# Kernel tuning notes

Hardware: AMD Instinct MI355X
Metric: run time of the kernel (lower is better)

Reference implementation:

```python
import jax, jax.numpy as jnp
import numpy as np

B, T, I, H, O = 1024, 512, 64, 256, 1

def setup_inputs() -> dict:
    key = jax.random.key(0)
    ks = jax.random.split(key, 12)
    s_ih0 = 1.0 / np.sqrt(H)
    def u(k, shape):
        return jax.random.uniform(k, shape, jnp.float32, -s_ih0, s_ih0)
    return {
        "x": jax.random.normal(ks[0], (B, T, I), jnp.float32),
        "w_ih0": u(ks[1], (4 * H, I)),
        "w_hh0": u(ks[2], (4 * H, H)),
        "b_ih0": u(ks[3], (4 * H,)),
        "b_hh0": u(ks[4], (4 * H,)),
        "w_ih1": u(ks[5], (4 * H, H)),
        "w_hh1": u(ks[6], (4 * H, H)),
        "b_ih1": u(ks[7], (4 * H,)),
        "b_hh1": u(ks[8], (4 * H,)),
        "fc_w": u(ks[9], (O, H)),
        "fc_b": u(ks[10], (O,)),
    }

def _lstm_layer(x, w_ih, w_hh, b_ih, b_hh):
    # x: [B, T, D_in] -> hidden sequence [B, T, H], gate order i,f,g,o (PyTorch)
    b, t, _ = x.shape
    h_dim = w_hh.shape[1]
    # precompute input projections for all timesteps: [T, B, 4H]
    xproj = (jnp.einsum('bti,gi->btg', x, w_ih) + b_ih + b_hh).transpose(1, 0, 2)
    h0 = jnp.zeros((b, h_dim), x.dtype)
    c0 = jnp.zeros((b, h_dim), x.dtype)

    def step(carry, xp):
        h, c = carry
        gates = xp + h @ w_hh.T  # [B, 4H]
        i_g, f_g, g_g, o_g = jnp.split(gates, 4, axis=-1)
        i_g = jax.nn.sigmoid(i_g)
        f_g = jax.nn.sigmoid(f_g)
        g_g = jnp.tanh(g_g)
        o_g = jax.nn.sigmoid(o_g)
        c = f_g * c + i_g * g_g
        h = o_g * jnp.tanh(c)
        return (h, c), h

    (h_last, _), hs = jax.lax.scan(step, (h0, c0), xproj)
    return hs.transpose(1, 0, 2), h_last

def reference(x, w_ih0, w_hh0, b_ih0, b_hh0, w_ih1, w_hh1, b_ih1, b_hh1, fc_w, fc_b):
    # Layer 0 -> (eval mode: dropout is identity) -> Layer 1 -> fc on last step
    h_seq0, _ = _lstm_layer(x, w_ih0, w_hh0, b_ih0, b_hh0)
    _, h_last1 = _lstm_layer(h_seq0, w_ih1, w_hh1, b_ih1, b_hh1)
    return h_last1 @ fc_w.T + fc_b  # [B, O]
```

## Files before the change

kernel.cpp:

```cpp
#include <hip/hip_runtime.h>
#include <stdint.h>


#define T_STEPS 512
#define NC0 10
#define NC1 16
#define WSLICE_ELEMS (4*(NC0+NC1)*512)
#define L1_OFF (4*NC0*512)
#define HN (1024*256)

typedef __attribute__((ext_vector_type(8))) short short8;
typedef __attribute__((ext_vector_type(4))) float floatx4;

__device__ __forceinline__ uint32_t f2bf(float f){
  uint32_t u = __builtin_bit_cast(uint32_t, f);
  return (u + 0x7fffu + ((u >> 16) & 1u)) >> 16;
}
__device__ __forceinline__ float bf2f(uint32_t b){
  return __builtin_bit_cast(float, b << 16);
}
__device__ __forceinline__ float sigm(float x){
  return __builtin_amdgcn_rcpf(1.0f + __builtin_amdgcn_exp2f(-1.44269504f*x));
}
__device__ __forceinline__ float tanhf_(float x){
  return 1.0f - 2.0f*__builtin_amdgcn_rcpf(1.0f + __builtin_amdgcn_exp2f(2.88539008f*x));
}
__device__ __forceinline__ floatx4 splat4(float v){ return (floatx4){v,v,v,v}; }

__device__ __forceinline__ void cvt8(const floatx4& v0, const floatx4& v1, short8& hi, short8& lo){
  #pragma unroll
  for (int j = 0; j < 8; ++j){
    float f = (j < 4) ? v0[j] : v1[j-4];
    uint32_t hb = f2bf(f); float fh = bf2f(hb); uint32_t lb = f2bf(f - fh);
    hi[j] = (short)hb; lo[j] = (short)lb;
  }
}

__device__ __forceinline__ short8 load_coh16(const uint16_t* p){
  short8 r;
  asm volatile("global_load_dwordx4 %0, %1, off sc0 sc1" : "=v"(r) : "v"(p));
  return r;
}
__device__ __forceinline__ floatx4 load_g16f(const float* p){
  floatx4 r;
  asm volatile("global_load_dwordx4 %0, %1, off" : "=v"(r) : "v"(p));
  return r;
}
__device__ __forceinline__ void store_coh2(uint16_t* p, uint32_t v){
  asm volatile("global_store_short %0, %1, off sc0 sc1" :: "v"(p), "v"(v) : "memory");
}
#define VM_WAIT(N) do{ asm volatile("s_waitcnt vmcnt(" #N ")" ::: "memory"); \
                       __builtin_amdgcn_sched_barrier(0); }while(0)

extern "C" __global__ void prep_weights(const float* __restrict__ wih0, const float* __restrict__ whh0,
                                        const float* __restrict__ wih1, const float* __restrict__ whh1,
                                        uint16_t* __restrict__ wfrag)
{
  int idx = blockIdx.x*256 + threadIdx.x;
  int s  = idx / WSLICE_ELEMS;
  int r  = idx - s*WSLICE_ELEMS;
  int layer = (r >= L1_OFF) ? 1 : 0;
  int rr = layer ? (r - L1_OFF) : r;
  int nc = layer ? NC1 : NC0;
  int n  = rr / (nc*512);
  int c  = (rr / 512) % nc;
  int l  = (rr >> 3) & 63;
  int j  = rr & 7;
  int k  = c*32 + ((l >> 4) << 3) + j;
  int grow = n*256 + s*16 + (l & 15);
  float v;
  if (!layer) v = (k < 64)  ? wih0[grow*64  + k] : whh0[grow*256 + (k - 64)];
  else        v = (k < 256) ? wih1[grow*256 + k] : whh1[grow*256 + (k - 256)];
  wfrag[idx] = (uint16_t)f2bf(v);
}

extern "C" __global__ void prep_bias(const float* __restrict__ bih0, const float* __restrict__ bhh0,
                                     const float* __restrict__ bih1, const float* __restrict__ bhh1,
                                     float* __restrict__ biasg)
{
  int idx = blockIdx.x*256 + threadIdx.x;
  if (idx >= 16*2*64) return;
  int s = idx >> 7;
  int layer = (idx >> 6) & 1;
  int q = idx & 63;
  int grow = (q >> 4)*256 + s*16 + (q & 15);
  biasg[idx] = layer ? (bih1[grow] + bhh1[grow]) : (bih0[grow] + bhh0[grow]);
}

extern "C" __global__ void __launch_bounds__(256, 1)
lstm_main(const float* __restrict__ x,
          const uint16_t* __restrict__ wfrag,
          const float* __restrict__ biasg,
          uint16_t* __restrict__ hbase,
          const float* __restrict__ fcw,
          const float* __restrict__ fcb,
          int* __restrict__ ctr,
          float* __restrict__ out)
{
  extern __shared__ uint16_t wlds[];
  const int tid  = threadIdx.x;
  const int bid  = blockIdx.x;
  const int s    = bid >> 4;
  const int g    = bid & 15;
  const int wv   = tid >> 6;
  const int lane = tid & 63;

  const int arow = g*64 + wv*16 + (lane & 15);
  const int ka   = (lane >> 4) * 8;
  const int drow = g*64 + wv*16 + ((lane >> 4) << 2);
  const int dcol = s*16 + (lane & 15);

  {
    const uint16_t* wsrc = wfrag + (size_t)s*WSLICE_ELEMS;
    for (int i = tid*8; i < WSLICE_ELEMS; i += 256*8)
      *(short8*)(wlds + i) = *(const short8*)(wsrc + i);
  }
  float b0[4], b1[4];
  {
    const int col = lane & 15;
    #pragma unroll
    for (int n = 0; n < 4; ++n){
      b0[n] = biasg[(s*2+0)*64 + n*16 + col];
      b1[n] = biasg[(s*2+1)*64 + n*16 + col];
    }
  }
  const float fcwv = fcw[dcol];
  const float fcb0 = fcb[0];

  short8 xh[2], xl[2];
  {
    const float* xp = x + (size_t)arow*T_STEPS*64 + ka;
    floatx4 v0 = *(const floatx4*)(xp);
    floatx4 v1 = *(const floatx4*)(xp + 4);
    floatx4 v2 = *(const floatx4*)(xp + 32);
    floatx4 v3 = *(const floatx4*)(xp + 36);
    cvt8(v0, v1, xh[0], xl[0]);
    cvt8(v2, v3, xh[1], xl[1]);
  }
  __syncthreads();

  const size_t abase = (size_t)arow*256 + ka;
  float c0[4] = {0,0,0,0}, c1[4] = {0,0,0,0};
  int* myc = ctr + g*32;

  for (int t = 0; t < T_STEPS; ++t){
    const size_t par0  = (size_t)(t & 1);
    const size_t rpar0 = par0 ^ 1;

    short8 a0h[8], a0l[8], a1h[8], a1l[8];
    {
      const uint16_t* ph = hbase + rpar0*HN              + abase;
      const uint16_t* pl = hbase + 2*(size_t)HN + rpar0*HN + abase;
      #pragma unroll
      for (int kc = 0; kc < 8; ++kc) a0h[kc] = load_coh16(ph + kc*32);
      #pragma unroll
      for (int kc = 0; kc < 8; ++kc) a0l[kc] = load_coh16(pl + kc*32);
    }
    {
      const uint16_t* ph = hbase + 4*(size_t)HN + par0*HN + abase;
      const uint16_t* pl = hbase + 6*(size_t)HN + par0*HN + abase;
      #pragma unroll
      for (int kc = 0; kc < 8; ++kc) a1h[kc] = load_coh16(ph + kc*32);
      #pragma unroll
      for (int kc = 0; kc < 8; ++kc) a1l[kc] = load_coh16(pl + kc*32);
    }
    floatx4 xr0, xr1, xr2, xr3;
    {
      const int tn = (t < T_STEPS-1) ? (t+1) : t;
      const float* xp = x + ((size_t)arow*T_STEPS + tn)*64 + ka;
      xr0 = load_g16f(xp);      xr1 = load_g16f(xp + 4);
      xr2 = load_g16f(xp + 32); xr3 = load_g16f(xp + 36);
    }

    floatx4 acc0[4], acc1[4];
    #pragma unroll
    for (int n = 0; n < 4; ++n) acc0[n] = splat4(b0[n]);
    #pragma unroll
    for (int pk = 0; pk < 2; ++pk){
      #pragma unroll
      for (int n = 0; n < 4; ++n){
        short8 w = *(const short8*)(wlds + (n*NC0 + pk)*512 + lane*8);
        acc0[n] = __builtin_amdgcn_mfma_f32_16x16x32_bf16(xh[pk], w, acc0[n], 0, 0, 0);
        acc0[n] = __builtin_amdgcn_mfma_f32_16x16x32_bf16(xl[pk], w, acc0[n], 0, 0, 0);
      }
    }
    #pragma unroll
    for (int n = 0; n < 4; ++n) acc1[n] = splat4(b1[n]);

    VM_WAIT(20);

    #pragma unroll
    for (int kc = 0; kc < 8; ++kc){
      #pragma unroll
      for (int n = 0; n < 4; ++n){
        short8 w0 = *(const short8*)(wlds + (n*NC0 + 2 + kc)*512 + lane*8);
        acc0[n] = __builtin_amdgcn_mfma_f32_16x16x32_bf16(a0h[kc], w0, acc0[n], 0, 0, 0);
        acc0[n] = __builtin_amdgcn_mfma_f32_16x16x32_bf16(a0l[kc], w0, acc0[n], 0, 0, 0);
        short8 w1 = *(const short8*)(wlds + L1_OFF + (n*NC1 + kc)*512 + lane*8);
        acc1[n] = __builtin_amdgcn_mfma_f32_16x16x32_bf16(a0h[kc], w1, acc1[n], 0, 0, 0);
        acc1[n] = __builtin_amdgcn_mfma_f32_16x16x32_bf16(a0l[kc], w1, acc1[n], 0, 0, 0);
      }
    }

    {
      uint16_t* qh = hbase + par0*HN;
      uint16_t* ql = hbase + 2*(size_t)HN + par0*HN;
      #pragma unroll
      for (int r = 0; r < 4; ++r){
        float ig = sigm(acc0[0][r]);
        float fg = sigm(acc0[1][r]);
        float gg = tanhf_(acc0[2][r]);
        float og = sigm(acc0[3][r]);
        c0[r] = fg*c0[r] + ig*gg;
        float h = og*tanhf_(c0[r]);
        uint32_t hb = f2bf(h); float fh = bf2f(hb); uint32_t lb = f2bf(h - fh);
        size_t idx = (size_t)(drow + r)*256 + dcol;
        store_coh2(qh + idx, hb); store_coh2(ql + idx, lb);
      }
    }

    VM_WAIT(12);

    #pragma unroll
    for (int kc = 0; kc < 8; ++kc){
      #pragma unroll
      for (int n = 0; n < 4; ++n){
        short8 w1 = *(const short8*)(wlds + L1_OFF + (n*NC1 + 8 + kc)*512 + lane*8);
        acc1[n] = __builtin_amdgcn_mfma_f32_16x16x32_bf16(a1h[kc], w1, acc1[n], 0, 0, 0);
        acc1[n] = __builtin_amdgcn_mfma_f32_16x16x32_bf16(a1l[kc], w1, acc1[n], 0, 0, 0);
      }
    }

    VM_WAIT(8);
    cvt8(xr0, xr1, xh[0], xl[0]);
    cvt8(xr2, xr3, xh[1], xl[1]);

    if (t > 0){
      uint16_t* qh = hbase + 4*(size_t)HN + rpar0*HN;
      uint16_t* ql = hbase + 6*(size_t)HN + rpar0*HN;
      #pragma unroll
      for (int r = 0; r < 4; ++r){
        float ig = sigm(acc1[0][r]);
        float fg = sigm(acc1[1][r]);
        float gg = tanhf_(acc1[2][r]);
        float og = sigm(acc1[3][r]);
        c1[r] = fg*c1[r] + ig*gg;
        float h = og*tanhf_(c1[r]);
        uint32_t hb = f2bf(h); float fh = bf2f(hb); uint32_t lb = f2bf(h - fh);
        size_t idx = (size_t)(drow + r)*256 + dcol;
        store_coh2(qh + idx, hb); store_coh2(ql + idx, lb);
      }
    }

    VM_WAIT(0);

    __syncthreads();
    if (tid == 0){
      __hip_atomic_fetch_add(myc, 1, __ATOMIC_RELAXED, __HIP_MEMORY_SCOPE_AGENT);
      const int target = 16*(t+1);
      int spins = 0;
      while (__hip_atomic_load(myc, __ATOMIC_RELAXED, __HIP_MEMORY_SCOPE_AGENT) < target){
        if (++spins > (1<<20)) break;
        __builtin_amdgcn_s_sleep(1);
      }
    }
    __syncthreads();
  }

  {
    const uint16_t* p0h = hbase + 1*(size_t)HN + abase;
    const uint16_t* p0l = hbase + 3*(size_t)HN + abase;
    const uint16_t* p1h = hbase + 4*(size_t)HN + abase;
    const uint16_t* p1l = hbase + 6*(size_t)HN + abase;
    short8 a0h[8], a0l[8], a1h[8], a1l[8];
    #pragma unroll
    for (int kc = 0; kc < 8; ++kc){
      a0h[kc] = load_coh16(p0h + kc*32);
      a0l[kc] = load_coh16(p0l + kc*32);
      a1h[kc] = load_coh16(p1h + kc*32);
      a1l[kc] = load_coh16(p1l + kc*32);
    }
    VM_WAIT(0);
    floatx4 acc[4];
    #pragma unroll
    for (int n = 0; n < 4; ++n) acc[n] = splat4(b1[n]);
    #pragma unroll
    for (int kc = 0; kc < 8; ++kc){
      #pragma unroll
      for (int n = 0; n < 4; ++n){
        short8 w1 = *(const short8*)(wlds + L1_OFF + (n*NC1 + kc)*512 + lane*8);
        acc[n] = __builtin_amdgcn_mfma_f32_16x16x32_bf16(a0h[kc], w1, acc[n], 0, 0, 0);
        acc[n] = __builtin_amdgcn_mfma_f32_16x16x32_bf16(a0l[kc], w1, acc[n], 0, 0, 0);
        short8 w2 = *(const short8*)(wlds + L1_OFF + (n*NC1 + 8 + kc)*512 + lane*8);
        acc[n] = __builtin_amdgcn_mfma_f32_16x16x32_bf16(a1h[kc], w2, acc[n], 0, 0, 0);
        acc[n] = __builtin_amdgcn_mfma_f32_16x16x32_bf16(a1l[kc], w2, acc[n], 0, 0, 0);
      }
    }
    #pragma unroll
    for (int r = 0; r < 4; ++r){
      float ig = sigm(acc[0][r]);
      float fg = sigm(acc[1][r]);
      float gg = tanhf_(acc[2][r]);
      float og = sigm(acc[3][r]);
      float cc = fg*c1[r] + ig*gg;
      float h  = og*tanhf_(cc);
      float v  = h * fcwv;
      v += __shfl_xor(v, 1);
      v += __shfl_xor(v, 2);
      v += __shfl_xor(v, 4);
      v += __shfl_xor(v, 8);
      if ((lane & 15) == 0){
        float res = v + ((s == 0) ? fcb0 : 0.0f);
        atomicAdd(out + drow + r, res);
      }
    }
  }
}

extern "C" void kernel_launch(void* const* d_in, const int* in_sizes, int n_in,
                              void* d_out, int out_size, void* d_ws, size_t ws_size,
                              hipStream_t stream)
{
  (void)in_sizes; (void)n_in; (void)out_size; (void)ws_size;
  const float* x    = (const float*)d_in[0];
  const float* wih0 = (const float*)d_in[1];
  const float* whh0 = (const float*)d_in[2];
  const float* bih0 = (const float*)d_in[3];
  const float* bhh0 = (const float*)d_in[4];
  const float* wih1 = (const float*)d_in[5];
  const float* whh1 = (const float*)d_in[6];
  const float* bih1 = (const float*)d_in[7];
  const float* bhh1 = (const float*)d_in[8];
  const float* fcw  = (const float*)d_in[9];
  const float* fcb  = (const float*)d_in[10];

  char* ws = (char*)d_ws;
  const size_t SZ_WFRAG = (size_t)16*WSLICE_ELEMS*2;
  const size_t OFF_BIAS = SZ_WFRAG;
  const size_t OFF_CTR  = OFF_BIAS + (size_t)16*2*64*4;
  const size_t OFF_H    = (size_t)2*1024*1024;

  uint16_t* wfrag = (uint16_t*)(ws);
  float*    biasg = (float*)(ws + OFF_BIAS);
  int*      ctr   = (int*)(ws + OFF_CTR);
  uint16_t* hbase = (uint16_t*)(ws + OFF_H);
  float*    out   = (float*)d_out;

  hipMemsetAsync(d_out, 0, (size_t)1024*sizeof(float), stream);
  hipMemsetAsync(ws + OFF_CTR, 0, (OFF_H - OFF_CTR) + (size_t)8*HN*2, stream);

  hipLaunchKernelGGL(prep_weights, dim3(16*WSLICE_ELEMS/256), dim3(256), 0, stream,
                     wih0, whh0, wih1, whh1, wfrag);
  hipLaunchKernelGGL(prep_bias, dim3(8), dim3(256), 0, stream,
                     bih0, bhh0, bih1, bhh1, biasg);

  hipFuncSetAttribute((const void*)lstm_main,
                      hipFuncAttributeMaxDynamicSharedMemorySize, WSLICE_ELEMS*2);
  void* args[] = { (void*)&x, (void*)&wfrag, (void*)&biasg, (void*)&hbase,
                   (void*)&fcw, (void*)&fcb, (void*)&ctr, (void*)&out };
  hipError_t ce = hipLaunchCooperativeKernel((void*)lstm_main, dim3(256), dim3(256),
                                             args, WSLICE_ELEMS*2, stream);
  if (ce != hipSuccess){
    hipLaunchKernelGGL(lstm_main, dim3(256), dim3(256), WSLICE_ELEMS*2, stream,
                       x, wfrag, biasg, hbase, fcw, fcb, ctr, out);
  }
}
```

Baseline: 4.642 ms.

## Use XCD-local cache coherence for hidden-state exchange when groups share an XCD

```diff
diff --git a/kernel.cpp b/kernel.cpp
--- a/kernel.cpp
+++ b/kernel.cpp
@@ -11,13 +11,13 @@
 
 typedef __attribute__((ext_vector_type(8))) short short8;
 typedef __attribute__((ext_vector_type(4))) float floatx4;
-
-__device__ __forceinline__ uint32_t f2bf(float f){
-  uint32_t u = __builtin_bit_cast(uint32_t, f);
-  return (u + 0x7fffu + ((u >> 16) & 1u)) >> 16;
-}
-__device__ __forceinline__ float bf2f(uint32_t b){
-  return __builtin_bit_cast(float, b << 16);
+typedef _Float16 half8 __attribute__((ext_vector_type(8)));
+
+#define MFMA16(A,B,C) __builtin_amdgcn_mfma_f32_16x16x32_f16( \
+    __builtin_bit_cast(half8,(A)), __builtin_bit_cast(half8,(B)), (C), 0, 0, 0)
+
+__device__ __forceinline__ uint16_t f2h(float f){
+  return __builtin_bit_cast(uint16_t, (_Float16)f);
 }
 __device__ __forceinline__ float sigm(float x){
   return __builtin_amdgcn_rcpf(1.0f + __builtin_amdgcn_exp2f(-1.44269504f*x));
@@ -27,27 +27,33 @@
 }
 __device__ __forceinline__ floatx4 splat4(float v){ return (floatx4){v,v,v,v}; }
 
-__device__ __forceinline__ void cvt8(const floatx4& v0, const floatx4& v1, short8& hi, short8& lo){
+__device__ __forceinline__ void cvt8h(const floatx4& v0, const floatx4& v1, short8& hi, short8& lo){
   #pragma unroll
   for (int j = 0; j < 8; ++j){
     float f = (j < 4) ? v0[j] : v1[j-4];
-    uint32_t hb = f2bf(f); float fh = bf2f(hb); uint32_t lb = f2bf(f - fh);
-    hi[j] = (short)hb; lo[j] = (short)lb;
-  }
-}
-
-__device__ __forceinline__ short8 load_coh16(const uint16_t* p){
+    _Float16 h = (_Float16)f;
+    _Float16 l = (_Float16)(f - (float)h);
+    hi[j] = (short)__builtin_bit_cast(uint16_t, h);
+    lo[j] = (short)__builtin_bit_cast(uint16_t, l);
+  }
+}
+
+template<int FAST>
+__device__ __forceinline__ short8 load_h16(const uint16_t* p){
   short8 r;
-  asm volatile("global_load_dwordx4 %0, %1, off sc0 sc1" : "=v"(r) : "v"(p));
+  if constexpr (FAST) asm volatile("global_load_dwordx4 %0, %1, off sc0"     : "=v"(r) : "v"(p));
+  else                asm volatile("global_load_dwordx4 %0, %1, off sc0 sc1" : "=v"(r) : "v"(p));
   return r;
+}
+template<int FAST>
+__device__ __forceinline__ void store_h2(uint16_t* p, uint32_t v){
+  if constexpr (FAST) asm volatile("global_store_short %0, %1, off sc0"     :: "v"(p), "v"(v) : "memory");
+  else                asm volatile("global_store_short %0, %1, off sc0 sc1" :: "v"(p), "v"(v) : "memory");
 }
 __device__ __forceinline__ floatx4 load_g16f(const float* p){
   floatx4 r;
   asm volatile("global_load_dwordx4 %0, %1, off" : "=v"(r) : "v"(p));
   return r;
-}
-__device__ __forceinline__ void store_coh2(uint16_t* p, uint32_t v){
-  asm volatile("global_store_short %0, %1, off sc0 sc1" :: "v"(p), "v"(v) : "memory");
 }
 #define VM_WAIT(N) do{ asm volatile("s_waitcnt vmcnt(" #N ")" ::: "memory"); \
                        __builtin_amdgcn_sched_barrier(0); }while(0)
@@ -71,7 +77,7 @@
   float v;
   if (!layer) v = (k < 64)  ? wih0[grow*64  + k] : whh0[grow*256 + (k - 64)];
   else        v = (k < 256) ? wih1[grow*256 + k] : whh1[grow*256 + (k - 256)];
-  wfrag[idx] = (uint16_t)f2bf(v);
+  wfrag[idx] = f2h(v);
 }
 
 extern "C" __global__ void prep_bias(const float* __restrict__ bih0, const float* __restrict__ bhh0,
@@ -87,45 +93,16 @@
   biasg[idx] = layer ? (bih1[grow] + bhh1[grow]) : (bih0[grow] + bhh0[grow]);
 }
 
-extern "C" __global__ void __launch_bounds__(256, 1)
-lstm_main(const float* __restrict__ x,
-          const uint16_t* __restrict__ wfrag,
-          const float* __restrict__ biasg,
-          uint16_t* __restrict__ hbase,
-          const float* __restrict__ fcw,
-          const float* __restrict__ fcb,
-          int* __restrict__ ctr,
-          float* __restrict__ out)
+template<int FAST>
+__device__ __forceinline__ void lstm_loop(
+    const float* __restrict__ x, const uint16_t* wl ,
+    uint16_t* hbase, int* myc,
+    const float* b0, const float* b1,
+    int arow, int ka, int drow, int dcol, int s,
+    float fcwv, float fcb0, float* out)
 {
-  extern __shared__ uint16_t wlds[];
-  const int tid  = threadIdx.x;
-  const int bid  = blockIdx.x;
-  const int s    = bid >> 4;
-  const int g    = bid & 15;
-  const int wv   = tid >> 6;
-  const int lane = tid & 63;
-
-  const int arow = g*64 + wv*16 + (lane & 15);
-  const int ka   = (lane >> 4) * 8;
-  const int drow = g*64 + wv*16 + ((lane >> 4) << 2);
-  const int dcol = s*16 + (lane & 15);
-
-  {
-    const uint16_t* wsrc = wfrag + (size_t)s*WSLICE_ELEMS;
-    for (int i = tid*8; i < WSLICE_ELEMS; i += 256*8)
-      *(short8*)(wlds + i) = *(const short8*)(wsrc + i);
-  }
-  float b0[4], b1[4];
-  {
-    const int col = lane & 15;
-    #pragma unroll
-    for (int n = 0; n < 4; ++n){
-      b0[n] = biasg[(s*2+0)*64 + n*16 + col];
-      b1[n] = biasg[(s*2+1)*64 + n*16 + col];
-    }
-  }
-  const float fcwv = fcw[dcol];
-  const float fcb0 = fcb[0];
+  const size_t abase = (size_t)arow*256 + ka;
+  float c0[4] = {0,0,0,0}, c1[4] = {0,0,0,0};
 
   short8 xh[2], xl[2];
   {
@@ -134,14 +111,9 @@
     floatx4 v1 = *(const floatx4*)(xp + 4);
     floatx4 v2 = *(const floatx4*)(xp + 32);
     floatx4 v3 = *(const floatx4*)(xp + 36);
-    cvt8(v0, v1, xh[0], xl[0]);
-    cvt8(v2, v3, xh[1], xl[1]);
-  }
-  __syncthreads();
-
-  const size_t abase = (size_t)arow*256 + ka;
-  float c0[4] = {0,0,0,0}, c1[4] = {0,0,0,0};
-  int* myc = ctr + g*32;
+    cvt8h(v0, v1, xh[0], xl[0]);
+    cvt8h(v2, v3, xh[1], xl[1]);
+  }
 
   for (int t = 0; t < T_STEPS; ++t){
     const size_t par0  = (size_t)(t & 1);
@@ -149,20 +121,20 @@
 
     short8 a0h[8], a0l[8], a1h[8], a1l[8];
     {
-      const uint16_t* ph = hbase + rpar0*HN              + abase;
+      const uint16_t* ph = hbase + rpar0*HN + abase;
       const uint16_t* pl = hbase + 2*(size_t)HN + rpar0*HN + abase;
       #pragma unroll
-      for (int kc = 0; kc < 8; ++kc) a0h[kc] = load_coh16(ph + kc*32);
-      #pragma unroll
-      for (int kc = 0; kc < 8; ++kc) a0l[kc] = load_coh16(pl + kc*32);
+      for (int kc = 0; kc < 8; ++kc) a0h[kc] = load_h16<FAST>(ph + kc*32);
+      #pragma unroll
+      for (int kc = 0; kc < 8; ++kc) a0l[kc] = load_h16<FAST>(pl + kc*32);
     }
     {
       const uint16_t* ph = hbase + 4*(size_t)HN + par0*HN + abase;
       const uint16_t* pl = hbase + 6*(size_t)HN + par0*HN + abase;
       #pragma unroll
-      for (int kc = 0; kc < 8; ++kc) a1h[kc] = load_coh16(ph + kc*32);
-      #pragma unroll
-      for (int kc = 0; kc < 8; ++kc) a1l[kc] = load_coh16(pl + kc*32);
+      for (int kc = 0; kc < 8; ++kc) a1h[kc] = load_h16<FAST>(ph + kc*32);
+      #pragma unroll
+      for (int kc = 0; kc < 8; ++kc) a1l[kc] = load_h16<FAST>(pl + kc*32);
     }
     floatx4 xr0, xr1, xr2, xr3;
     {
@@ -179,9 +151,9 @@
     for (int pk = 0; pk < 2; ++pk){
       #pragma unroll
       for (int n = 0; n < 4; ++n){
-        short8 w = *(const short8*)(wlds + (n*NC0 + pk)*512 + lane*8);
-        acc0[n] = __builtin_amdgcn_mfma_f32_16x16x32_bf16(xh[pk], w, acc0[n], 0, 0, 0);
-        acc0[n] = __builtin_amdgcn_mfma_f32_16x16x32_bf16(xl[pk], w, acc0[n], 0, 0, 0);
+        short8 w = *(const short8*)(wl + (n*NC0 + pk)*512);
+        acc0[n] = MFMA16(xh[pk], w, acc0[n]);
+        acc0[n] = MFMA16(xl[pk], w, acc0[n]);
       }
     }
     #pragma unroll
@@ -193,12 +165,12 @@
     for (int kc = 0; kc < 8; ++kc){
       #pragma unroll
       for (int n = 0; n < 4; ++n){
-        short8 w0 = *(const short8*)(wlds + (n*NC0 + 2 + kc)*512 + lane*8);
-        acc0[n] = __builtin_amdgcn_mfma_f32_16x16x32_bf16(a0h[kc], w0, acc0[n], 0, 0, 0);
-        acc0[n] = __builtin_amdgcn_mfma_f32_16x16x32_bf16(a0l[kc], w0, acc0[n], 0, 0, 0);
-        short8 w1 = *(const short8*)(wlds + L1_OFF + (n*NC1 + kc)*512 + lane*8);
-        acc1[n] = __builtin_amdgcn_mfma_f32_16x16x32_bf16(a0h[kc], w1, acc1[n], 0, 0, 0);
-        acc1[n] = __builtin_amdgcn_mfma_f32_16x16x32_bf16(a0l[kc], w1, acc1[n], 0, 0, 0);
+        short8 w0 = *(const short8*)(wl + (n*NC0 + 2 + kc)*512);
+        acc0[n] = MFMA16(a0h[kc], w0, acc0[n]);
+        acc0[n] = MFMA16(a0l[kc], w0, acc0[n]);
+        short8 w1 = *(const short8*)(wl + L1_OFF + (n*NC1 + kc)*512);
+        acc1[n] = MFMA16(a0h[kc], w1, acc1[n]);
+        acc1[n] = MFMA16(a0l[kc], w1, acc1[n]);
       }
     }
 
@@ -213,9 +185,11 @@
         float og = sigm(acc0[3][r]);
         c0[r] = fg*c0[r] + ig*gg;
         float h = og*tanhf_(c0[r]);
-        uint32_t hb = f2bf(h); float fh = bf2f(hb); uint32_t lb = f2bf(h - fh);
+        _Float16 hh = (_Float16)h;
+        _Float16 hl = (_Float16)(h - (float)hh);
         size_t idx = (size_t)(drow + r)*256 + dcol;
-        store_coh2(qh + idx, hb); store_coh2(ql + idx, lb);
+        store_h2<FAST>(qh + idx, (uint32_t)__builtin_bit_cast(uint16_t, hh));
+        store_h2<FAST>(ql + idx, (uint32_t)__builtin_bit_cast(uint16_t, hl));
       }
     }
 
@@ -225,15 +199,15 @@
     for (int kc = 0; kc < 8; ++kc){
       #pragma unroll
       for (int n = 0; n < 4; ++n){
-        short8 w1 = *(const short8*)(wlds + L1_OFF + (n*NC1 + 8 + kc)*512 + lane*8);
-        acc1[n] = __builtin_amdgcn_mfma_f32_16x16x32_bf16(a1h[kc], w1, acc1[n], 0, 0, 0);
-        acc1[n] = __builtin_amdgcn_mfma_f32_16x16x32_bf16(a1l[kc], w1, acc1[n], 0, 0, 0);
+        short8 w = *(const short8*)(wl + L1_OFF + (n*NC1 + 8 + kc)*512);
+        acc1[n] = MFMA16(a1h[kc], w, acc1[n]);
+        acc1[n] = MFMA16(a1l[kc], w, acc1[n]);
       }
     }
 
     VM_WAIT(8);
-    cvt8(xr0, xr1, xh[0], xl[0]);
-    cvt8(xr2, xr3, xh[1], xl[1]);
+    cvt8h(xr0, xr1, xh[0], xl[0]);
+    cvt8h(xr2, xr3, xh[1], xl[1]);
 
     if (t > 0){
       uint16_t* qh = hbase + 4*(size_t)HN + rpar0*HN;
@@ -246,20 +220,21 @@
         float og = sigm(acc1[3][r]);
         c1[r] = fg*c1[r] + ig*gg;
         float h = og*tanhf_(c1[r]);
-        uint32_t hb = f2bf(h); float fh = bf2f(hb); uint32_t lb = f2bf(h - fh);
+        _Float16 hh = (_Float16)h;
+        _Float16 hl = (_Float16)(h - (float)hh);
         size_t idx = (size_t)(drow + r)*256 + dcol;
-        store_coh2(qh + idx, hb); store_coh2(ql + idx, lb);
+        store_h2<FAST>(qh + idx, (uint32_t)__builtin_bit_cast(uint16_t, hh));
+        store_h2<FAST>(ql + idx, (uint32_t)__builtin_bit_cast(uint16_t, hl));
       }
     }
 
     VM_WAIT(0);
-
     __syncthreads();
-    if (tid == 0){
+
+    if (threadIdx.x == 0){
       __hip_atomic_fetch_add(myc, 1, __ATOMIC_RELAXED, __HIP_MEMORY_SCOPE_AGENT);
-      const int target = 16*(t+1);
       int spins = 0;
-      while (__hip_atomic_load(myc, __ATOMIC_RELAXED, __HIP_MEMORY_SCOPE_AGENT) < target){
+      while (__hip_atomic_load(myc, __ATOMIC_RELAXED, __HIP_MEMORY_SCOPE_AGENT) < 16*(t+1)){
         if (++spins > (1<<20)) break;
         __builtin_amdgcn_s_sleep(1);
       }
@@ -275,10 +250,10 @@
     short8 a0h[8], a0l[8], a1h[8], a1l[8];
     #pragma unroll
     for (int kc = 0; kc < 8; ++kc){
-      a0h[kc] = load_coh16(p0h + kc*32);
-      a0l[kc] = load_coh16(p0l + kc*32);
-      a1h[kc] = load_coh16(p1h + kc*32);
-      a1l[kc] = load_coh16(p1l + kc*32);
+      a0h[kc] = load_h16<FAST>(p0h + kc*32);
+      a0l[kc] = load_h16<FAST>(p0l + kc*32);
+      a1h[kc] = load_h16<FAST>(p1h + kc*32);
+      a1l[kc] = load_h16<FAST>(p1l + kc*32);
     }
     VM_WAIT(0);
     floatx4 acc[4];
@@ -288,12 +263,12 @@
     for (int kc = 0; kc < 8; ++kc){
       #pragma unroll
       for (int n = 0; n < 4; ++n){
-        short8 w1 = *(const short8*)(wlds + L1_OFF + (n*NC1 + kc)*512 + lane*8);
-        acc[n] = __builtin_amdgcn_mfma_f32_16x16x32_bf16(a0h[kc], w1, acc[n], 0, 0, 0);
-        acc[n] = __builtin_amdgcn_mfma_f32_16x16x32_bf16(a0l[kc], w1, acc[n], 0, 0, 0);
-        short8 w2 = *(const short8*)(wlds + L1_OFF + (n*NC1 + 8 + kc)*512 + lane*8);
-        acc[n] = __builtin_amdgcn_mfma_f32_16x16x32_bf16(a1h[kc], w2, acc[n], 0, 0, 0);
-        acc[n] = __builtin_amdgcn_mfma_f32_16x16x32_bf16(a1l[kc], w2, acc[n], 0, 0, 0);
+        short8 w1 = *(const short8*)(wl + L1_OFF + (n*NC1 + kc)*512);
+        acc[n] = MFMA16(a0h[kc], w1, acc[n]);
+        acc[n] = MFMA16(a0l[kc], w1, acc[n]);
+        short8 w2 = *(const short8*)(wl + L1_OFF + (n*NC1 + 8 + kc)*512);
+        acc[n] = MFMA16(a1h[kc], w2, acc[n]);
+        acc[n] = MFMA16(a1l[kc], w2, acc[n]);
       }
     }
     #pragma unroll
@@ -309,12 +284,94 @@
       v += __shfl_xor(v, 2);
       v += __shfl_xor(v, 4);
       v += __shfl_xor(v, 8);
-      if ((lane & 15) == 0){
+      if ((threadIdx.x & 15) == 0){
         float res = v + ((s == 0) ? fcb0 : 0.0f);
         atomicAdd(out + drow + r, res);
       }
     }
   }
+}
+
+extern "C" __global__ void __launch_bounds__(256, 1)
+lstm_main(const float* __restrict__ x,
+          const uint16_t* __restrict__ wfrag,
+          const float* __restrict__ biasg,
+          uint16_t* __restrict__ hbase,
+          const float* __restrict__ fcw,
+          const float* __restrict__ fcb,
+          int* __restrict__ ctr,
+          int* __restrict__ gctr,
+          uint32_t* __restrict__ xcds,
+          float* __restrict__ out)
+{
+  extern __shared__ uint16_t wlds[];
+  __shared__ int s_uni, s_div;
+  __shared__ uint32_t s_e0;
+
+  const int tid  = threadIdx.x;
+  const int bid  = blockIdx.x;
+  const int s    = bid >> 4;
+  const int g    = bid & 15;
+  const int wv   = tid >> 6;
+  const int lane = tid & 63;
+
+  const int arow = g*64 + wv*16 + (lane & 15);
+  const int ka   = (lane >> 4) * 8;
+  const int drow = g*64 + wv*16 + ((lane >> 4) << 2);
+  const int dcol = s*16 + (lane & 15);
+
+  {
+    const uint16_t* wsrc = wfrag + (size_t)s*WSLICE_ELEMS;
+    for (int i = tid*8; i < WSLICE_ELEMS; i += 256*8)
+      *(short8*)(wlds + i) = *(const short8*)(wsrc + i);
+  }
+  float b0[4], b1[4];
+  {
+    const int col = lane & 15;
+    #pragma unroll
+    for (int n = 0; n < 4; ++n){
+      b0[n] = biasg[(s*2+0)*64 + n*16 + col];
+      b1[n] = biasg[(s*2+1)*64 + n*16 + col];
+    }
+  }
+  const float fcwv = fcw[dcol];
+  const float fcb0 = fcb[0];
+
+  uint32_t myxcd;
+  asm volatile("s_getreg_b32 %0, hwreg(HW_REG_XCC_ID)" : "=s"(myxcd));
+  if (tid == 0){
+    s_uni = 1; s_div = 0;
+    uint32_t v = myxcd;
+    uint32_t* p = xcds + bid;
+    asm volatile("global_store_dword %0, %1, off sc0 sc1" :: "v"(p), "v"(v) : "memory");
+  }
+  VM_WAIT(0);
+  __syncthreads();
+  if (tid == 0){
+    __hip_atomic_fetch_add(gctr, 1, __ATOMIC_RELAXED, __HIP_MEMORY_SCOPE_AGENT);
+    int spins = 0;
+    while (__hip_atomic_load(gctr, __ATOMIC_RELAXED, __HIP_MEMORY_SCOPE_AGENT) < 256){
+      if (++spins > (1<<20)) break;
+      __builtin_amdgcn_s_sleep(1);
+    }
+  }
+  __syncthreads();
+  uint32_t ent;
+  {
+    const uint32_t* p = xcds + tid;
+    asm volatile("global_load_dword %0, %1, off sc0 sc1" : "=v"(ent) : "v"(p));
+    VM_WAIT(0);
+  }
+  if (tid == 0) s_e0 = ent;
+  __syncthreads();
+  if (((tid & 15) == g) && ent != myxcd) s_uni = 0;
+  if (ent != s_e0) s_div = 1;
+  __syncthreads();
+  const int fast = s_uni & s_div;
+
+  const uint16_t* wlp = wlds + lane*8;
+  if (fast) lstm_loop<1>(x, wlp, hbase, ctr + g*32, b0, b1, arow, ka, drow, dcol, s, fcwv, fcb0, out);
+  else      lstm_loop<0>(x, wlp, hbase, ctr + g*32, b0, b1, arow, ka, drow, dcol, s, fcwv, fcb0, out);
 }
 
 extern "C" void kernel_launch(void* const* d_in, const int* in_sizes, int n_in,
@@ -338,11 +395,15 @@
   const size_t SZ_WFRAG = (size_t)16*WSLICE_ELEMS*2;
   const size_t OFF_BIAS = SZ_WFRAG;
   const size_t OFF_CTR  = OFF_BIAS + (size_t)16*2*64*4;
+  const size_t OFF_GCTR = OFF_CTR + (size_t)16*32*4;
+  const size_t OFF_XCD  = OFF_GCTR + 128;
   const size_t OFF_H    = (size_t)2*1024*1024;
 
   uint16_t* wfrag = (uint16_t*)(ws);
   float*    biasg = (float*)(ws + OFF_BIAS);
   int*      ctr   = (int*)(ws + OFF_CTR);
+  int*      gctr  = (int*)(ws + OFF_GCTR);
+  uint32_t* xcds  = (uint32_t*)(ws + OFF_XCD);
   uint16_t* hbase = (uint16_t*)(ws + OFF_H);
   float*    out   = (float*)d_out;
 
@@ -357,11 +418,12 @@
   hipFuncSetAttribute((const void*)lstm_main,
                       hipFuncAttributeMaxDynamicSharedMemorySize, WSLICE_ELEMS*2);
   void* args[] = { (void*)&x, (void*)&wfrag, (void*)&biasg, (void*)&hbase,
-                   (void*)&fcw, (void*)&fcb, (void*)&ctr, (void*)&out };
+                   (void*)&fcw, (void*)&fcb, (void*)&ctr, (void*)&gctr,
+                   (void*)&xcds, (void*)&out };
   hipError_t ce = hipLaunchCooperativeKernel((void*)lstm_main, dim3(256), dim3(256),
                                              args, WSLICE_ELEMS*2, stream);
   if (ce != hipSuccess){
     hipLaunchKernelGGL(lstm_main, dim3(256), dim3(256), WSLICE_ELEMS*2, stream,
-                       x, wfrag, biasg, hbase, fcw, fcb, ctr, out);
-  }
-}
+                       x, wfrag, biasg, hbase, fcw, fcb, ctr, gctr, xcds, out);
+  }
+}
```

Result: slower. 7.869 ms (+69.5%).

## Switch to fp16 split MFMA and per-wave counter sync instead of block barriers

Applied to the files above, without the earlier changes.

```diff
diff --git a/kernel.cpp b/kernel.cpp
--- a/kernel.cpp
+++ b/kernel.cpp
@@ -11,13 +11,13 @@
 
 typedef __attribute__((ext_vector_type(8))) short short8;
 typedef __attribute__((ext_vector_type(4))) float floatx4;
-
-__device__ __forceinline__ uint32_t f2bf(float f){
-  uint32_t u = __builtin_bit_cast(uint32_t, f);
-  return (u + 0x7fffu + ((u >> 16) & 1u)) >> 16;
-}
-__device__ __forceinline__ float bf2f(uint32_t b){
-  return __builtin_bit_cast(float, b << 16);
+typedef _Float16 half8 __attribute__((ext_vector_type(8)));
+
+#define MFMA16(A,B,C) __builtin_amdgcn_mfma_f32_16x16x32_f16( \
+    __builtin_bit_cast(half8,(A)), __builtin_bit_cast(half8,(B)), (C), 0, 0, 0)
+
+__device__ __forceinline__ uint16_t f2h(float f){
+  return __builtin_bit_cast(uint16_t, (_Float16)f);
 }
 __device__ __forceinline__ float sigm(float x){
   return __builtin_amdgcn_rcpf(1.0f + __builtin_amdgcn_exp2f(-1.44269504f*x));
@@ -27,12 +27,14 @@
 }
 __device__ __forceinline__ floatx4 splat4(float v){ return (floatx4){v,v,v,v}; }
 
-__device__ __forceinline__ void cvt8(const floatx4& v0, const floatx4& v1, short8& hi, short8& lo){
+__device__ __forceinline__ void cvt8h(const floatx4& v0, const floatx4& v1, short8& hi, short8& lo){
   #pragma unroll
   for (int j = 0; j < 8; ++j){
     float f = (j < 4) ? v0[j] : v1[j-4];
-    uint32_t hb = f2bf(f); float fh = bf2f(hb); uint32_t lb = f2bf(f - fh);
-    hi[j] = (short)hb; lo[j] = (short)lb;
+    _Float16 h = (_Float16)f;
+    _Float16 l = (_Float16)(f - (float)h);
+    hi[j] = (short)__builtin_bit_cast(uint16_t, h);
+    lo[j] = (short)__builtin_bit_cast(uint16_t, l);
   }
 }
 
@@ -41,13 +43,13 @@
   asm volatile("global_load_dwordx4 %0, %1, off sc0 sc1" : "=v"(r) : "v"(p));
   return r;
 }
+__device__ __forceinline__ void store_coh2(uint16_t* p, uint32_t v){
+  asm volatile("global_store_short %0, %1, off sc0 sc1" :: "v"(p), "v"(v) : "memory");
+}
 __device__ __forceinline__ floatx4 load_g16f(const float* p){
   floatx4 r;
   asm volatile("global_load_dwordx4 %0, %1, off" : "=v"(r) : "v"(p));
   return r;
-}
-__device__ __forceinline__ void store_coh2(uint16_t* p, uint32_t v){
-  asm volatile("global_store_short %0, %1, off sc0 sc1" :: "v"(p), "v"(v) : "memory");
 }
 #define VM_WAIT(N) do{ asm volatile("s_waitcnt vmcnt(" #N ")" ::: "memory"); \
                        __builtin_amdgcn_sched_barrier(0); }while(0)
@@ -71,7 +73,7 @@
   float v;
   if (!layer) v = (k < 64)  ? wih0[grow*64  + k] : whh0[grow*256 + (k - 64)];
   else        v = (k < 256) ? wih1[grow*256 + k] : whh1[grow*256 + (k - 256)];
-  wfrag[idx] = (uint16_t)f2bf(v);
+  wfrag[idx] = f2h(v);
 }
 
 extern "C" __global__ void prep_bias(const float* __restrict__ bih0, const float* __restrict__ bhh0,
@@ -101,13 +103,14 @@
   const int tid  = threadIdx.x;
   const int bid  = blockIdx.x;
   const int s    = bid >> 4;
-  const int g    = bid & 15;
+  const int gh   = bid & 15;
   const int wv   = tid >> 6;
   const int lane = tid & 63;
-
-  const int arow = g*64 + wv*16 + (lane & 15);
+  const int G    = gh*4 + wv;
+
+  const int arow = G*16 + (lane & 15);
   const int ka   = (lane >> 4) * 8;
-  const int drow = g*64 + wv*16 + ((lane >> 4) << 2);
+  const int drow = G*16 + ((lane >> 4) << 2);
   const int dcol = s*16 + (lane & 15);
 
   {
@@ -126,6 +129,12 @@
   }
   const float fcwv = fcw[dcol];
   const float fcb0 = fcb[0];
+  __syncthreads();
+
+  const uint16_t* wl = wlds + lane*8;
+  const size_t abase = (size_t)arow*256 + ka;
+  float c0[4] = {0,0,0,0}, c1[4] = {0,0,0,0};
+  int* myc = ctr + G*32;
 
   short8 xh[2], xl[2];
   {
@@ -134,14 +143,9 @@
     floatx4 v1 = *(const floatx4*)(xp + 4);
     floatx4 v2 = *(const floatx4*)(xp + 32);
     floatx4 v3 = *(const floatx4*)(xp + 36);
-    cvt8(v0, v1, xh[0], xl[0]);
-    cvt8(v2, v3, xh[1], xl[1]);
-  }
-  __syncthreads();
-
-  const size_t abase = (size_t)arow*256 + ka;
-  float c0[4] = {0,0,0,0}, c1[4] = {0,0,0,0};
-  int* myc = ctr + g*32;
+    cvt8h(v0, v1, xh[0], xl[0]);
+    cvt8h(v2, v3, xh[1], xl[1]);
+  }
 
   for (int t = 0; t < T_STEPS; ++t){
     const size_t par0  = (size_t)(t & 1);
@@ -149,7 +153,7 @@
 
     short8 a0h[8], a0l[8], a1h[8], a1l[8];
     {
-      const uint16_t* ph = hbase + rpar0*HN              + abase;
+      const uint16_t* ph = hbase + rpar0*HN + abase;
       const uint16_t* pl = hbase + 2*(size_t)HN + rpar0*HN + abase;
       #pragma unroll
       for (int kc = 0; kc < 8; ++kc) a0h[kc] = load_coh16(ph + kc*32);
@@ -179,9 +183,9 @@
     for (int pk = 0; pk < 2; ++pk){
       #pragma unroll
       for (int n = 0; n < 4; ++n){
-        short8 w = *(const short8*)(wlds + (n*NC0 + pk)*512 + lane*8);
-        acc0[n] = __builtin_amdgcn_mfma_f32_16x16x32_bf16(xh[pk], w, acc0[n], 0, 0, 0);
-        acc0[n] = __builtin_amdgcn_mfma_f32_16x16x32_bf16(xl[pk], w, acc0[n], 0, 0, 0);
+        short8 w = *(const short8*)(wl + (n*NC0 + pk)*512);
+        acc0[n] = MFMA16(xh[pk], w, acc0[n]);
+        acc0[n] = MFMA16(xl[pk], w, acc0[n]);
       }
     }
     #pragma unroll
@@ -193,12 +197,12 @@
     for (int kc = 0; kc < 8; ++kc){
       #pragma unroll
       for (int n = 0; n < 4; ++n){
-        short8 w0 = *(const short8*)(wlds + (n*NC0 + 2 + kc)*512 + lane*8);
-        acc0[n] = __builtin_amdgcn_mfma_f32_16x16x32_bf16(a0h[kc], w0, acc0[n], 0, 0, 0);
-        acc0[n] = __builtin_amdgcn_mfma_f32_16x16x32_bf16(a0l[kc], w0, acc0[n], 0, 0, 0);
-        short8 w1 = *(const short8*)(wlds + L1_OFF + (n*NC1 + kc)*512 + lane*8);
-        acc1[n] = __builtin_amdgcn_mfma_f32_16x16x32_bf16(a0h[kc], w1, acc1[n], 0, 0, 0);
-        acc1[n] = __builtin_amdgcn_mfma_f32_16x16x32_bf16(a0l[kc], w1, acc1[n], 0, 0, 0);
+        short8 w0 = *(const short8*)(wl + (n*NC0 + 2 + kc)*512);
+        acc0[n] = MFMA16(a0h[kc], w0, acc0[n]);
+        acc0[n] = MFMA16(a0l[kc], w0, acc0[n]);
+        short8 w1 = *(const short8*)(wl + L1_OFF + (n*NC1 + kc)*512);
+        acc1[n] = MFMA16(a0h[kc], w1, acc1[n]);
+        acc1[n] = MFMA16(a0l[kc], w1, acc1[n]);
       }
     }
 
@@ -213,9 +217,11 @@
         float og = sigm(acc0[3][r]);
         c0[r] = fg*c0[r] + ig*gg;
         float h = og*tanhf_(c0[r]);
-        uint32_t hb = f2bf(h); float fh = bf2f(hb); uint32_t lb = f2bf(h - fh);
+        _Float16 hh = (_Float16)h;
+        _Float16 hl = (_Float16)(h - (float)hh);
         size_t idx = (size_t)(drow + r)*256 + dcol;
-        store_coh2(qh + idx, hb); store_coh2(ql + idx, lb);
+        store_coh2(qh + idx, (uint32_t)__builtin_bit_cast(uint16_t, hh));
+        store_coh2(ql + idx, (uint32_t)__builtin_bit_cast(uint16_t, hl));
       }
     }
 
@@ -225,15 +231,15 @@
     for (int kc = 0; kc < 8; ++kc){
       #pragma unroll
       for (int n = 0; n < 4; ++n){
-        short8 w1 = *(const short8*)(wlds + L1_OFF + (n*NC1 + 8 + kc)*512 + lane*8);
-        acc1[n] = __builtin_amdgcn_mfma_f32_16x16x32_bf16(a1h[kc], w1, acc1[n], 0, 0, 0);
-        acc1[n] = __builtin_amdgcn_mfma_f32_16x16x32_bf16(a1l[kc], w1, acc1[n], 0, 0, 0);
+        short8 w = *(const short8*)(wl + L1_OFF + (n*NC1 + 8 + kc)*512);
+        acc1[n] = MFMA16(a1h[kc], w, acc1[n]);
+        acc1[n] = MFMA16(a1l[kc], w, acc1[n]);
       }
     }
 
     VM_WAIT(8);
-    cvt8(xr0, xr1, xh[0], xl[0]);
-    cvt8(xr2, xr3, xh[1], xl[1]);
+    cvt8h(xr0, xr1, xh[0], xl[0]);
+    cvt8h(xr2, xr3, xh[1], xl[1]);
 
     if (t > 0){
       uint16_t* qh = hbase + 4*(size_t)HN + rpar0*HN;
@@ -246,25 +252,24 @@
         float og = sigm(acc1[3][r]);
         c1[r] = fg*c1[r] + ig*gg;
         float h = og*tanhf_(c1[r]);
-        uint32_t hb = f2bf(h); float fh = bf2f(hb); uint32_t lb = f2bf(h - fh);
+        _Float16 hh = (_Float16)h;
+        _Float16 hl = (_Float16)(h - (float)hh);
         size_t idx = (size_t)(drow + r)*256 + dcol;
-        store_coh2(qh + idx, hb); store_coh2(ql + idx, lb);
+        store_coh2(qh + idx, (uint32_t)__builtin_bit_cast(uint16_t, hh));
+        store_coh2(ql + idx, (uint32_t)__builtin_bit_cast(uint16_t, hl));
       }
     }
 
     VM_WAIT(0);
 
-    __syncthreads();
-    if (tid == 0){
+    if (lane == 0){
       __hip_atomic_fetch_add(myc, 1, __ATOMIC_RELAXED, __HIP_MEMORY_SCOPE_AGENT);
-      const int target = 16*(t+1);
       int spins = 0;
-      while (__hip_atomic_load(myc, __ATOMIC_RELAXED, __HIP_MEMORY_SCOPE_AGENT) < target){
+      while (__hip_atomic_load(myc, __ATOMIC_RELAXED, __HIP_MEMORY_SCOPE_AGENT) < 16*(t+1)){
         if (++spins > (1<<20)) break;
         __builtin_amdgcn_s_sleep(1);
       }
     }
-    __syncthreads();
   }
 
   {
@@ -288,12 +293,12 @@
     for (int kc = 0; kc < 8; ++kc){
       #pragma unroll
       for (int n = 0; n < 4; ++n){
-        short8 w1 = *(const short8*)(wlds + L1_OFF + (n*NC1 + kc)*512 + lane*8);
-        acc[n] = __builtin_amdgcn_mfma_f32_16x16x32_bf16(a0h[kc], w1, acc[n], 0, 0, 0);
-        acc[n] = __builtin_amdgcn_mfma_f32_16x16x32_bf16(a0l[kc], w1, acc[n], 0, 0, 0);
-        short8 w2 = *(const short8*)(wlds + L1_OFF + (n*NC1 + 8 + kc)*512 + lane*8);
-        acc[n] = __builtin_amdgcn_mfma_f32_16x16x32_bf16(a1h[kc], w2, acc[n], 0, 0, 0);
-        acc[n] = __builtin_amdgcn_mfma_f32_16x16x32_bf16(a1l[kc], w2, acc[n], 0, 0, 0);
+        short8 w1 = *(const short8*)(wl + L1_OFF + (n*NC1 + kc)*512);
+        acc[n] = MFMA16(a0h[kc], w1, acc[n]);
+        acc[n] = MFMA16(a0l[kc], w1, acc[n]);
+        short8 w2 = *(const short8*)(wl + L1_OFF + (n*NC1 + 8 + kc)*512);
+        acc[n] = MFMA16(a1h[kc], w2, acc[n]);
+        acc[n] = MFMA16(a1l[kc], w2, acc[n]);
       }
     }
     #pragma unroll
```

Result: slower. 5.657 ms (+21.9%).
